# Kernel tuning notes

Measured on AMD Instinct MI355X. Metric: run time of the kernel, lower is better.

The kernel has to match this reference:

```python
import jax, jax.numpy as jnp
import numpy as np

N_ATOMS = 50000
ATOM_FDIM = 133
HIDDEN = 128
DEPTH = 3
N_EDGES = 800000
N_MOLS = 1024
BN_EPS = 1e-5


def setup_inputs() -> dict:
    key = jax.random.key(0)
    ks = jax.random.split(key, 10)
    f_atoms = jax.random.normal(ks[0], (N_ATOMS, ATOM_FDIM), dtype=jnp.float32)
    W_in = jax.random.normal(ks[1], (ATOM_FDIM, HIDDEN), dtype=jnp.float32) / np.sqrt(ATOM_FDIM)
    b_in = jax.random.normal(ks[2], (HIDDEN,), dtype=jnp.float32) * 0.01
    W1 = jax.random.normal(ks[3], (DEPTH, HIDDEN, HIDDEN), dtype=jnp.float32) / np.sqrt(HIDDEN)
    b1 = jax.random.normal(ks[4], (DEPTH, HIDDEN), dtype=jnp.float32) * 0.01
    W2 = jax.random.normal(ks[5], (DEPTH, HIDDEN, HIDDEN), dtype=jnp.float32) / np.sqrt(HIDDEN)
    b2 = jax.random.normal(ks[6], (DEPTH, HIDDEN), dtype=jnp.float32) * 0.01
    gamma = jnp.ones((DEPTH, HIDDEN), dtype=jnp.float32)
    beta = jnp.zeros((DEPTH, HIDDEN), dtype=jnp.float32)
    eps_param = jnp.zeros((DEPTH,), dtype=jnp.float32)
    edge_index = jax.random.randint(ks[7], (2, N_EDGES), 0, N_ATOMS, dtype=jnp.int64 if jax.config.jax_enable_x64 else jnp.int32).astype(jnp.int32)
    segment_ids = jnp.sort(jax.random.randint(ks[8], (N_ATOMS,), 0, N_MOLS).astype(jnp.int32))
    return {"f_atoms": f_atoms, "W_in": W_in, "b_in": b_in, "W1": W1, "b1": b1,
            "W2": W2, "b2": b2, "gamma": gamma, "beta": beta, "eps_param": eps_param,
            "edge_index": edge_index, "segment_ids": segment_ids}


def _gin_forward(f_atoms, W_in, b_in, W1, b1, W2, b2, gamma, beta, eps_param,
                 edge_index, segment_ids):
    src, tgt = edge_index[0], edge_index[1]
    # input projection + ReLU
    x = jax.nn.relu(f_atoms @ W_in + b_in)  # [N, H]
    for d in range(DEPTH):
        # scatter-add of gathered neighbor features + (1+eps) self term
        agg = jnp.zeros_like(x).at[tgt].add(x[src]) + (1.0 + eps_param[d]) * x
        h = jax.nn.relu(agg @ W1[d] + b1[d])
        h = h @ W2[d] + b2[d]
        # BatchNorm1d (training-mode batch statistics)
        mean = jnp.mean(h, axis=0)
        var = jnp.var(h, axis=0)
        h = gamma[d] * (h - mean) * jax.lax.rsqrt(var + BN_EPS) + beta[d]
        x = jax.nn.relu(h)
    # per-molecule mean pooling (a_scope -> segment mean); empty mols -> zeros
    sums = jax.ops.segment_sum(x, segment_ids, num_segments=N_MOLS)  # [M, H]
    counts = jax.ops.segment_sum(jnp.ones((x.shape[0],), x.dtype), segment_ids,
                                 num_segments=N_MOLS)
    mol_vecs = jnp.where(counts[:, None] > 0, sums / jnp.maximum(counts, 1.0)[:, None], 0.0)
    return mol_vecs


def reference(f_atoms, W_in, b_in, W1, b1, W2, b2, gamma, beta, eps_param,
              edge_index, segment_ids):
    return _gin_forward(f_atoms, W_in, b_in, W1, b1, W2, b2, gamma, beta,
                        eps_param, edge_index, segment_ids)
```

## Files before the change

kernel.cpp:

```cpp
#include <hip/hip_runtime.h>
#include <hip/hip_fp16.h>

#define N_ATOMS   50000
#define ATOM_FDIM 133
#define HIDDEN    128
#define DEPTH     3
#define N_EDGES   800000
#define N_MOLS    1024
#define BN_EPS    1e-5f
#define K_IN_PAD  160
#define BUCKET    64

typedef _Float16 f16x8 __attribute__((ext_vector_type(8)));
typedef float    f32x4 __attribute__((ext_vector_type(4)));

struct __align__(8) half4pack { __half2 a, b; };

#define LDS_S 40

__global__ void setup_kernel(const float* __restrict__ f,
                             const float* __restrict__ W_in,
                             const float* __restrict__ W1,
                             const float* __restrict__ W2,
                             const int* __restrict__ seg,
                             __half* __restrict__ Ah, __half* __restrict__ Wt,
                             float* __restrict__ stats, int* __restrict__ moloff,
                             int* __restrict__ wcur)
{
    const int NCH = N_ATOMS * (K_IN_PAD / 4);
    const int NW4 = (128 * K_IN_PAD + 2 * DEPTH * 128 * 128) / 4;
    int i = blockIdx.x * 256 + threadIdx.x;
    if (i < NCH) {
        int row = i / (K_IN_PAD / 4);
        int c4  = (i - row * (K_IN_PAD / 4)) * 4;
        float v[4];
        #pragma unroll
        for (int u = 0; u < 4; ++u) {
            int k = c4 + u;
            v[u] = (k < ATOM_FDIM) ? f[(size_t)row * ATOM_FDIM + k] : 0.f;
        }
        half4pack p;
        p.a = __float22half2_rn(make_float2(v[0], v[1]));
        p.b = __float22half2_rn(make_float2(v[2], v[3]));
        *(half4pack*)&Ah[(size_t)row * K_IN_PAD + c4] = p;
        return;
    }
    int j = i - NCH;
    if (j < NW4) {
        float v[4];
        #pragma unroll
        for (int u = 0; u < 4; ++u) {
            int e = j * 4 + u;
            if (e < 128 * K_IN_PAD) {
                int n = e / K_IN_PAD, k = e - n * K_IN_PAD;
                v[u] = (k < ATOM_FDIM) ? W_in[(size_t)k * 128 + n] : 0.f;
            } else if (e < 128 * K_IN_PAD + DEPTH * 128 * 128) {
                int q = e - 128 * K_IN_PAD;
                int d = q >> 14, r = q & 16383;
                int n = r >> 7, k = r & 127;
                v[u] = W1[((size_t)d * 128 + k) * 128 + n];
            } else {
                int q = e - 128 * K_IN_PAD - DEPTH * 128 * 128;
                int d = q >> 14, r = q & 16383;
                int n = r >> 7, k = r & 127;
                v[u] = W2[((size_t)d * 128 + k) * 128 + n];
            }
        }
        half4pack p;
        p.a = __float22half2_rn(make_float2(v[0], v[1]));
        p.b = __float22half2_rn(make_float2(v[2], v[3]));
        *(half4pack*)&Wt[j * 4] = p;
        return;
    }
    int m = j - NCH >= 0 ? j - NW4 : 0;
    m = j - NW4;
    if (m < DEPTH * 256) stats[m] = 0.f;
    if (m >= 0 && m <= N_MOLS) {
        int lo = 0, hi = N_ATOMS;
        while (lo < hi) {
            int mid = (lo + hi) >> 1;
            if (seg[mid] < m) lo = mid + 1; else hi = mid;
        }
        moloff[m] = lo;
    }
    if (m >= 0 && m < N_ATOMS / 4) ((int4*)wcur)[m] = make_int4(0, 0, 0, 0);
}

#define FILLB ((N_EDGES / 4 + 255) / 256)
#define GB    ((N_ATOMS + 127) / 128)

__global__ __launch_bounds__(256, 2) void fill_proj(
    const int* __restrict__ src, const int* __restrict__ tgt,
    int* __restrict__ wcur, unsigned short* __restrict__ col,
    const __half* __restrict__ A, const __half* __restrict__ Bt,
    const float* __restrict__ bias, __half* __restrict__ C)
{
    __shared__ __align__(16) __half As[128 * LDS_S];
    __shared__ __align__(16) __half Bs[128 * LDS_S];

    if (blockIdx.x < FILLB) {
        int e4 = (blockIdx.x * 256 + threadIdx.x) * 4;
        if (e4 < N_EDGES) {
            int4 t4 = *(const int4*)&tgt[e4];
            int4 s4 = *(const int4*)&src[e4];
            int p0 = atomicAdd(&wcur[t4.x], 1);
            int p1 = atomicAdd(&wcur[t4.y], 1);
            int p2 = atomicAdd(&wcur[t4.z], 1);
            int p3 = atomicAdd(&wcur[t4.w], 1);
            if (p0 < BUCKET) col[(size_t)t4.x * BUCKET + p0] = (unsigned short)s4.x;
            if (p1 < BUCKET) col[(size_t)t4.y * BUCKET + p1] = (unsigned short)s4.y;
            if (p2 < BUCKET) col[(size_t)t4.z * BUCKET + p2] = (unsigned short)s4.z;
            if (p3 < BUCKET) col[(size_t)t4.w * BUCKET + p3] = (unsigned short)s4.w;
        }
        return;
    }

    const int t = threadIdx.x;
    const int w = t >> 6, lane = t & 63;
    const int wm = w >> 1, wn = w & 1;
    const int l15 = lane & 15, quad = lane >> 4;
    const int row0 = (blockIdx.x - FILLB) * 128;
    const int M = N_ATOMS, K = K_IN_PAD;

    f32x4 acc[4][4];
    #pragma unroll
    for (int mt = 0; mt < 4; ++mt)
        #pragma unroll
        for (int nt = 0; nt < 4; ++nt) acc[mt][nt] = (f32x4){0.f, 0.f, 0.f, 0.f};

    for (int k0 = 0; k0 < K; k0 += 32) {
        #pragma unroll
        for (int i = 0; i < 2; ++i) {
            int c = t * 2 + i;
            int r = c >> 2, o = c & 3;
            int row = row0 + r;
            uint4 v = make_uint4(0, 0, 0, 0);
            if (row < M) v = *(const uint4*)&A[(size_t)row * K + k0 + o * 8];
            *(uint4*)&As[r * LDS_S + o * 8] = v;
        }
        #pragma unroll
        for (int i = 0; i < 2; ++i) {
            int c = t * 2 + i;
            int r = c >> 2, o = c & 3;
            uint4 v = *(const uint4*)&Bt[(size_t)r * K + k0 + o * 8];
            *(uint4*)&Bs[r * LDS_S + o * 8] = v;
        }
        __syncthreads();
        f16x8 af[4], bf[4];
        #pragma unroll
        for (int mt = 0; mt < 4; ++mt)
            af[mt] = *(const f16x8*)&As[(wm * 64 + mt * 16 + l15) * LDS_S + quad * 8];
        #pragma unroll
        for (int nt = 0; nt < 4; ++nt)
            bf[nt] = *(const f16x8*)&Bs[(wn * 64 + nt * 16 + l15) * LDS_S + quad * 8];
        #pragma unroll
        for (int mt = 0; mt < 4; ++mt)
            #pragma unroll
            for (int nt = 0; nt < 4; ++nt)
                acc[mt][nt] = __builtin_amdgcn_mfma_f32_16x16x32_f16(af[mt], bf[nt], acc[mt][nt], 0, 0, 0);
        __syncthreads();
    }

    #pragma unroll
    for (int nt = 0; nt < 4; ++nt) {
        int cc = wn * 64 + nt * 16 + l15;
        float b = bias[cc];
        #pragma unroll
        for (int mt = 0; mt < 4; ++mt) {
            #pragma unroll
            for (int r = 0; r < 4; ++r) {
                int row = row0 + wm * 64 + mt * 16 + quad * 4 + r;
                if (row < M) {
                    float o = fmaxf(acc[mt][nt][r] + b, 0.f);
                    C[(size_t)row * 128 + cc] = __float2half(o);
                }
            }
        }
    }
}

template<bool BN>
__global__ __launch_bounds__(256) void aggregate_kernel(
    const __half2* __restrict__ xh2, const int* __restrict__ cnt,
    const unsigned short* __restrict__ col, const float* __restrict__ eps_param, int d,
    const float* __restrict__ s1, const float* __restrict__ s2,
    const float* __restrict__ gamma, const float* __restrict__ beta, int dprev,
    __half2* __restrict__ aggh2)
{
    int gw = (blockIdx.x * 256 + threadIdx.x) >> 6;
    int lane = threadIdx.x & 63;
    float e1 = 1.0f + eps_param[d];

    float2 sc = make_float2(0.f, 0.f), sh = make_float2(0.f, 0.f);
    if (BN) {
        const float inv_n = 1.0f / (float)N_ATOMS;
        int c0 = lane * 2;
        float m0 = s1[c0] * inv_n;
        float v0 = fmaxf(s2[c0] * inv_n - m0 * m0, 0.f);
        float m1 = s1[c0 + 1] * inv_n;
        float v1 = fmaxf(s2[c0 + 1] * inv_n - m1 * m1, 0.f);
        sc.x = gamma[dprev * 128 + c0]     * rsqrtf(v0 + BN_EPS);
        sc.y = gamma[dprev * 128 + c0 + 1] * rsqrtf(v1 + BN_EPS);
        sh.x = beta[dprev * 128 + c0]     - m0 * sc.x;
        sh.y = beta[dprev * 128 + c0 + 1] - m1 * sc.y;
    }

    float2 a = __half22float2(xh2[(size_t)gw * 64 + lane]);
    if (BN) {
        a.x = fmaxf(a.x * sc.x + sh.x, 0.f);
        a.y = fmaxf(a.y * sc.y + sh.y, 0.f);
    }
    float2 acc;
    acc.x = a.x * e1;
    acc.y = a.y * e1;

    int n = min(cnt[gw], BUCKET);
    const unsigned short* bp = &col[(size_t)gw * BUCKET];
    for (int i = 0; i < n; i += 8) {
        #pragma unroll
        for (int u = 0; u < 8; ++u) {
            int idx = i + u;
            int c = bp[min(idx, n - 1)];
            float2 f = __half22float2(xh2[(size_t)c * 64 + lane]);
            if (BN) {
                f.x = fmaxf(f.x * sc.x + sh.x, 0.f);
                f.y = fmaxf(f.y * sc.y + sh.y, 0.f);
            }
            if (idx < n) {
                acc.x += f.x;
                acc.y += f.y;
            }
        }
    }
    aggh2[(size_t)gw * 64 + lane] = __float22half2_rn(acc);
}

__global__ __launch_bounds__(256, 2) void mlp_fused(
    const __half* __restrict__ A, const __half* __restrict__ B1t,
    const __half* __restrict__ B2t,
    const float* __restrict__ bias1, const float* __restrict__ bias2,
    __half* __restrict__ C, int M,
    float* __restrict__ s1, float* __restrict__ s2)
{
    __shared__ __align__(16) __half As[4 * 128 * LDS_S];
    __shared__ __align__(16) __half Bs[4 * 128 * LDS_S];

    const int t = threadIdx.x;
    const int w = t >> 6, lane = t & 63;
    const int wm = w >> 1, wn = w & 1;
    const int l15 = lane & 15, quad = lane >> 4;
    const int row0 = blockIdx.x * 128;

    f32x4 acc[4][4];
    #pragma unroll
    for (int mt = 0; mt < 4; ++mt)
        #pragma unroll
        for (int nt = 0; nt < 4; ++nt) acc[mt][nt] = (f32x4){0.f, 0.f, 0.f, 0.f};

    #pragma unroll
    for (int i = 0; i < 8; ++i) {
        int c = i * 256 + t;
        int r = c >> 4, o = c & 15;
        int kc = o >> 2, oo = o & 3;
        int row = row0 + r;
        uint4 v = make_uint4(0, 0, 0, 0);
        if (row < M) v = *(const uint4*)&A[(size_t)row * 128 + o * 8];
        *(uint4*)&As[(kc * 128 + r) * LDS_S + oo * 8] = v;
    }
    #pragma unroll
    for (int i = 0; i < 8; ++i) {
        int c = i * 256 + t;
        int r = c >> 4, o = c & 15;
        int kc = o >> 2, oo = o & 3;
        uint4 v = *(const uint4*)&B1t[(size_t)r * 128 + o * 8];
        *(uint4*)&Bs[(kc * 128 + r) * LDS_S + oo * 8] = v;
    }
    __syncthreads();

    #pragma unroll
    for (int kc = 0; kc < 4; ++kc) {
        f16x8 af[4], bf[4];
        #pragma unroll
        for (int mt = 0; mt < 4; ++mt)
            af[mt] = *(const f16x8*)&As[(kc * 128 + wm * 64 + mt * 16 + l15) * LDS_S + quad * 8];
        #pragma unroll
        for (int nt = 0; nt < 4; ++nt)
            bf[nt] = *(const f16x8*)&Bs[(kc * 128 + wn * 64 + nt * 16 + l15) * LDS_S + quad * 8];
        #pragma unroll
        for (int mt = 0; mt < 4; ++mt)
            #pragma unroll
            for (int nt = 0; nt < 4; ++nt)
                acc[mt][nt] = __builtin_amdgcn_mfma_f32_16x16x32_f16(af[mt], bf[nt], acc[mt][nt], 0, 0, 0);
    }
    __syncthreads();

    #pragma unroll
    for (int nt = 0; nt < 4; ++nt) {
        int k = wn * 64 + nt * 16 + l15;
        float b = bias1[k];
        int kc = k >> 5, ko = k & 31;
        #pragma unroll
        for (int mt = 0; mt < 4; ++mt) {
            #pragma unroll
            for (int r = 0; r < 4; ++r) {
                int rl = wm * 64 + mt * 16 + quad * 4 + r;
                float h = fmaxf(acc[mt][nt][r] + b, 0.f);
                As[(kc * 128 + rl) * LDS_S + ko] = __float2half(h);
            }
        }
    }
    #pragma unroll
    for (int i = 0; i < 8; ++i) {
        int c = i * 256 + t;
        int r = c >> 4, o = c & 15;
        int kc = o >> 2, oo = o & 3;
        uint4 v = *(const uint4*)&B2t[(size_t)r * 128 + o * 8];
        *(uint4*)&Bs[(kc * 128 + r) * LDS_S + oo * 8] = v;
    }
    __syncthreads();

    #pragma unroll
    for (int mt = 0; mt < 4; ++mt)
        #pragma unroll
        for (int nt = 0; nt < 4; ++nt) acc[mt][nt] = (f32x4){0.f, 0.f, 0.f, 0.f};
    #pragma unroll
    for (int kc = 0; kc < 4; ++kc) {
        f16x8 af[4], bf[4];
        #pragma unroll
        for (int mt = 0; mt < 4; ++mt)
            af[mt] = *(const f16x8*)&As[(kc * 128 + wm * 64 + mt * 16 + l15) * LDS_S + quad * 8];
        #pragma unroll
        for (int nt = 0; nt < 4; ++nt)
            bf[nt] = *(const f16x8*)&Bs[(kc * 128 + wn * 64 + nt * 16 + l15) * LDS_S + quad * 8];
        #pragma unroll
        for (int mt = 0; mt < 4; ++mt)
            #pragma unroll
            for (int nt = 0; nt < 4; ++nt)
                acc[mt][nt] = __builtin_amdgcn_mfma_f32_16x16x32_f16(af[mt], bf[nt], acc[mt][nt], 0, 0, 0);
    }

    float ps[4] = {0, 0, 0, 0}, pss[4] = {0, 0, 0, 0};
    #pragma unroll
    for (int nt = 0; nt < 4; ++nt) {
        int cc = wn * 64 + nt * 16 + l15;
        float b = bias2[cc];
        #pragma unroll
        for (int mt = 0; mt < 4; ++mt) {
            #pragma unroll
            for (int r = 0; r < 4; ++r) {
                int row = row0 + wm * 64 + mt * 16 + quad * 4 + r;
                if (row < M) {
                    float o = acc[mt][nt][r] + b;
                    ps[nt] += o;
                    pss[nt] += o * o;
                    C[(size_t)row * 128 + cc] = __float2half(o);
                }
            }
        }
    }

    float* red1 = (float*)As;
    float* red2 = (float*)Bs;
    int contrib = wm * 4 + quad;
    __syncthreads();
    #pragma unroll
    for (int nt = 0; nt < 4; ++nt) {
        int cc = wn * 64 + nt * 16 + l15;
        red1[contrib * 128 + cc] = ps[nt];
        red2[contrib * 128 + cc] = pss[nt];
    }
    __syncthreads();
    if (t < 128) {
        float s = 0.f, q = 0.f;
        #pragma unroll
        for (int g = 0; g < 8; ++g) {
            s += red1[g * 128 + t];
            q += red2[g * 128 + t];
        }
        atomicAdd(&s1[t], s);
        atomicAdd(&s2[t], q);
    }
}

__global__ void pool_kernel(const __half* __restrict__ hh, const int* __restrict__ off,
                            const float* __restrict__ s1, const float* __restrict__ s2,
                            const float* __restrict__ gamma, const float* __restrict__ beta,
                            int dprev, float* __restrict__ out)
{
    int m = blockIdx.x;
    int c = threadIdx.x;
    const float inv_n = 1.0f / (float)N_ATOMS;
    float mean = s1[c] * inv_n;
    float var = fmaxf(s2[c] * inv_n - mean * mean, 0.f);
    float sc = gamma[dprev * 128 + c] * rsqrtf(var + BN_EPS);
    float sh = beta[dprev * 128 + c] - mean * sc;
    int s = off[m], e = off[m + 1];
    float acc = 0.f;
    for (int r = s; r < e; ++r) {
        float v = __half2float(hh[(size_t)r * 128 + c]);
        acc += fmaxf(v * sc + sh, 0.f);
    }
    int cnt = e - s;
    out[m * 128 + c] = (cnt > 0) ? acc / (float)cnt : 0.f;
}

extern "C" void kernel_launch(void* const* d_in, const int* in_sizes, int n_in,
                              void* d_out, int out_size, void* d_ws, size_t ws_size,
                              hipStream_t stream)
{
    const float* f_atoms   = (const float*)d_in[0];
    const float* W_in      = (const float*)d_in[1];
    const float* b_in      = (const float*)d_in[2];
    const float* W1        = (const float*)d_in[3];
    const float* b1        = (const float*)d_in[4];
    const float* W2        = (const float*)d_in[5];
    const float* b2        = (const float*)d_in[6];
    const float* gamma     = (const float*)d_in[7];
    const float* beta      = (const float*)d_in[8];
    const float* eps_param = (const float*)d_in[9];
    const int*   edge_index= (const int*)d_in[10];
    const int*   seg       = (const int*)d_in[11];
    const int*   src = edge_index;
    const int*   tgt = edge_index + N_EDGES;
    float* out = (float*)d_out;

    char* ws = (char*)d_ws;
    size_t off = 0;
    auto alloc = [&](size_t bytes) -> char* {
        char* p = ws + off;
        off += (bytes + 255) & ~(size_t)255;
        return p;
    };
    __half* xh    = (__half*)alloc((size_t)N_ATOMS * HIDDEN * 2);
    __half* aggh  = (__half*)alloc((size_t)N_ATOMS * HIDDEN * 2);
    __half* hpre  = (__half*)alloc((size_t)N_ATOMS * HIDDEN * 2);
    __half* Ah    = (__half*)alloc((size_t)N_ATOMS * K_IN_PAD * 2);
    __half* Wt    = (__half*)alloc((size_t)(128 * K_IN_PAD + 2 * DEPTH * 128 * 128) * 2);
    int*   wcur   = (int*)alloc(N_ATOMS * 4);
    unsigned short* col = (unsigned short*)alloc((size_t)N_ATOMS * BUCKET * 2);
    float* s12    = (float*)alloc(DEPTH * 256 * 4);
    int*   moloff = (int*)alloc((N_MOLS + 1) * 4);

    const __half* Wt_in = Wt;
    const __half* W1t   = Wt + 128 * K_IN_PAD;
    const __half* W2t   = W1t + DEPTH * 128 * 128;

    {
        const int NCH = N_ATOMS * (K_IN_PAD / 4);
        const int NW4 = (128 * K_IN_PAD + 2 * DEPTH * 128 * 128) / 4;
        const int TOT = NCH + NW4 + N_ATOMS / 4;
        setup_kernel<<<(TOT + 255) / 256, 256, 0, stream>>>(
            f_atoms, W_in, W1, W2, seg, Ah, Wt, s12, moloff, wcur);
    }

    fill_proj<<<FILLB + GB, 256, 0, stream>>>(src, tgt, wcur, col, Ah, Wt_in, b_in, xh);

    for (int d = 0; d < DEPTH; ++d) {
        float* s1d = s12 + d * 256;
        float* s2d = s1d + 128;
        if (d == 0) {
            aggregate_kernel<false><<<N_ATOMS / 4, 256, 0, stream>>>(
                (const __half2*)xh, wcur, col, eps_param, d,
                nullptr, nullptr, nullptr, nullptr, 0, (__half2*)aggh);
        } else {
            float* s1p = s12 + (d - 1) * 256;
            float* s2p = s1p + 128;
            aggregate_kernel<true><<<N_ATOMS / 4, 256, 0, stream>>>(
                (const __half2*)hpre, wcur, col, eps_param, d,
                s1p, s2p, gamma, beta, d - 1, (__half2*)aggh);
        }
        mlp_fused<<<GB, 256, 0, stream>>>(
            aggh, W1t + (size_t)d * 128 * 128, W2t + (size_t)d * 128 * 128,
            b1 + d * HIDDEN, b2 + d * HIDDEN, hpre, N_ATOMS, s1d, s2d);
    }

    pool_kernel<<<N_MOLS, 128, 0, stream>>>(
        hpre, moloff, s12 + (DEPTH - 1) * 256, s12 + (DEPTH - 1) * 256 + 128,
        gamma, beta, DEPTH - 1, out);
}
```

Baseline: 359.0 us.

## Fuse fp32-to-fp16 atom feature conversion into input projection GEMM loads

Removes the separate setup pass that converted and padded f_atoms into a half-precision staging buffer. The projection GEMM now reads the fp32 features directly, masks the padding columns, and converts to fp16 while filling LDS. This saves one full write and reread of the padded feature matrix. The edge bucketing also moves from four edges per thread to one, and the GEMM blocks are now placed before the fill blocks in the grid. The trade-off is that the GEMM does scalar, unaligned fp32 loads (row stride 133) instead of 16-byte vector loads.

```diff
diff --git a/kernel.cpp b/kernel.cpp
--- a/kernel.cpp
+++ b/kernel.cpp
@@ -18,34 +18,16 @@
 
 #define LDS_S 40
 
-__global__ void setup_kernel(const float* __restrict__ f,
-                             const float* __restrict__ W_in,
+__global__ void setup_kernel(const float* __restrict__ W_in,
                              const float* __restrict__ W1,
                              const float* __restrict__ W2,
                              const int* __restrict__ seg,
-                             __half* __restrict__ Ah, __half* __restrict__ Wt,
+                             __half* __restrict__ Wt,
                              float* __restrict__ stats, int* __restrict__ moloff,
                              int* __restrict__ wcur)
 {
-    const int NCH = N_ATOMS * (K_IN_PAD / 4);
     const int NW4 = (128 * K_IN_PAD + 2 * DEPTH * 128 * 128) / 4;
-    int i = blockIdx.x * 256 + threadIdx.x;
-    if (i < NCH) {
-        int row = i / (K_IN_PAD / 4);
-        int c4  = (i - row * (K_IN_PAD / 4)) * 4;
-        float v[4];
-        #pragma unroll
-        for (int u = 0; u < 4; ++u) {
-            int k = c4 + u;
-            v[u] = (k < ATOM_FDIM) ? f[(size_t)row * ATOM_FDIM + k] : 0.f;
-        }
-        half4pack p;
-        p.a = __float22half2_rn(make_float2(v[0], v[1]));
-        p.b = __float22half2_rn(make_float2(v[2], v[3]));
-        *(half4pack*)&Ah[(size_t)row * K_IN_PAD + c4] = p;
-        return;
-    }
-    int j = i - NCH;
+    int j = blockIdx.x * 256 + threadIdx.x;
     if (j < NW4) {
         float v[4];
         #pragma unroll
@@ -72,10 +54,9 @@
         *(half4pack*)&Wt[j * 4] = p;
         return;
     }
-    int m = j - NCH >= 0 ? j - NW4 : 0;
-    m = j - NW4;
+    int m = j - NW4;
     if (m < DEPTH * 256) stats[m] = 0.f;
-    if (m >= 0 && m <= N_MOLS) {
+    if (m <= N_MOLS) {
         int lo = 0, hi = N_ATOMS;
         while (lo < hi) {
             int mid = (lo + hi) >> 1;
@@ -83,34 +64,28 @@
         }
         moloff[m] = lo;
     }
-    if (m >= 0 && m < N_ATOMS / 4) ((int4*)wcur)[m] = make_int4(0, 0, 0, 0);
-}
-
-#define FILLB ((N_EDGES / 4 + 255) / 256)
+    if (m < N_ATOMS / 4) ((int4*)wcur)[m] = make_int4(0, 0, 0, 0);
+}
+
 #define GB    ((N_ATOMS + 127) / 128)
+#define FILLB ((N_EDGES + 255) / 256)
 
 __global__ __launch_bounds__(256, 2) void fill_proj(
     const int* __restrict__ src, const int* __restrict__ tgt,
     int* __restrict__ wcur, unsigned short* __restrict__ col,
-    const __half* __restrict__ A, const __half* __restrict__ Bt,
+    const float* __restrict__ f, const __half* __restrict__ Bt,
     const float* __restrict__ bias, __half* __restrict__ C)
 {
     __shared__ __align__(16) __half As[128 * LDS_S];
     __shared__ __align__(16) __half Bs[128 * LDS_S];
 
-    if (blockIdx.x < FILLB) {
-        int e4 = (blockIdx.x * 256 + threadIdx.x) * 4;
-        if (e4 < N_EDGES) {
-            int4 t4 = *(const int4*)&tgt[e4];
-            int4 s4 = *(const int4*)&src[e4];
-            int p0 = atomicAdd(&wcur[t4.x], 1);
-            int p1 = atomicAdd(&wcur[t4.y], 1);
-            int p2 = atomicAdd(&wcur[t4.z], 1);
-            int p3 = atomicAdd(&wcur[t4.w], 1);
-            if (p0 < BUCKET) col[(size_t)t4.x * BUCKET + p0] = (unsigned short)s4.x;
-            if (p1 < BUCKET) col[(size_t)t4.y * BUCKET + p1] = (unsigned short)s4.y;
-            if (p2 < BUCKET) col[(size_t)t4.z * BUCKET + p2] = (unsigned short)s4.z;
-            if (p3 < BUCKET) col[(size_t)t4.w * BUCKET + p3] = (unsigned short)s4.w;
+    if (blockIdx.x >= GB) {
+        int e = (blockIdx.x - GB) * 256 + threadIdx.x;
+        if (e < N_EDGES) {
+            int tg = tgt[e];
+            int sv = src[e];
+            int p = atomicAdd(&wcur[tg], 1);
+            if (p < BUCKET) col[(size_t)tg * BUCKET + p] = (unsigned short)sv;
         }
         return;
     }
@@ -119,7 +94,7 @@
     const int w = t >> 6, lane = t & 63;
     const int wm = w >> 1, wn = w & 1;
     const int l15 = lane & 15, quad = lane >> 4;
-    const int row0 = (blockIdx.x - FILLB) * 128;
+    const int row0 = blockIdx.x * 128;
     const int M = N_ATOMS, K = K_IN_PAD;
 
     f32x4 acc[4][4];
@@ -134,9 +109,15 @@
             int c = t * 2 + i;
             int r = c >> 2, o = c & 3;
             int row = row0 + r;
-            uint4 v = make_uint4(0, 0, 0, 0);
-            if (row < M) v = *(const uint4*)&A[(size_t)row * K + k0 + o * 8];
-            *(uint4*)&As[r * LDS_S + o * 8] = v;
+            int kb = k0 + o * 8;
+            __half h8[8];
+            #pragma unroll
+            for (int u = 0; u < 8; ++u) {
+                int k = kb + u;
+                float v = (row < M && k < ATOM_FDIM) ? f[(size_t)row * ATOM_FDIM + k] : 0.f;
+                h8[u] = __float2half(v);
+            }
+            *(uint4*)&As[r * LDS_S + o * 8] = *(uint4*)h8;
         }
         #pragma unroll
         for (int i = 0; i < 2; ++i) {
@@ -434,7 +415,6 @@
     __half* xh    = (__half*)alloc((size_t)N_ATOMS * HIDDEN * 2);
     __half* aggh  = (__half*)alloc((size_t)N_ATOMS * HIDDEN * 2);
     __half* hpre  = (__half*)alloc((size_t)N_ATOMS * HIDDEN * 2);
-    __half* Ah    = (__half*)alloc((size_t)N_ATOMS * K_IN_PAD * 2);
     __half* Wt    = (__half*)alloc((size_t)(128 * K_IN_PAD + 2 * DEPTH * 128 * 128) * 2);
     int*   wcur   = (int*)alloc(N_ATOMS * 4);
     unsigned short* col = (unsigned short*)alloc((size_t)N_ATOMS * BUCKET * 2);
@@ -446,14 +426,13 @@
     const __half* W2t   = W1t + DEPTH * 128 * 128;
 
     {
-        const int NCH = N_ATOMS * (K_IN_PAD / 4);
         const int NW4 = (128 * K_IN_PAD + 2 * DEPTH * 128 * 128) / 4;
-        const int TOT = NCH + NW4 + N_ATOMS / 4;
+        const int TOT = NW4 + N_ATOMS / 4;
         setup_kernel<<<(TOT + 255) / 256, 256, 0, stream>>>(
-            f_atoms, W_in, W1, W2, seg, Ah, Wt, s12, moloff, wcur);
-    }
-
-    fill_proj<<<FILLB + GB, 256, 0, stream>>>(src, tgt, wcur, col, Ah, Wt_in, b_in, xh);
+            W_in, W1, W2, seg, Wt, s12, moloff, wcur);
+    }
+
+    fill_proj<<<GB + FILLB, 256, 0, stream>>>(src, tgt, wcur, col, f_atoms, Wt_in, b_in, xh);
 
     for (int d = 0; d < DEPTH; ++d) {
         float* s1d = s12 + d * 256;
```

Result: no change. 357.5 us (-0.4%).
